# Kernel tuning notes

Hardware: AMD Instinct MI355X
Metric: run time of the kernel (lower is better)

## Reference

```python
import jax, jax.numpy as jnp
import numpy as np

_LOG2PI = float(np.log(2.0 * np.pi))


def setup_inputs() -> dict:
    key = jax.random.key(0)
    ks = jax.random.split(key, 9)
    B, T, S, A, O = 64, 128, 512, 16, 4096
    regime = jax.random.randint(ks[0], (B,), 0, 2).astype(jnp.float32)
    obs = jax.random.randint(ks[1], (T + 1, B), 0, O, dtype=jnp.int32)
    rewards = jax.random.normal(ks[2], (T + 1, B), jnp.float32)
    dones = jnp.zeros((T + 1, B), jnp.float32)
    actions = jax.random.randint(ks[3], (T, B), 0, A, dtype=jnp.int32)
    prior_logits = jax.random.normal(ks[4], (S,), jnp.float32)
    trans_logits = jax.random.normal(ks[5], (A, S, S), jnp.float32)
    obs_logits = jax.random.normal(ks[6], (S, O), jnp.float32)
    policy_logits = jax.random.normal(ks[7], (S, A), jnp.float32)
    r_mu = jax.random.normal(ks[8], (S,), jnp.float32)
    r_logsig = jnp.zeros((S,), jnp.float32)
    return {"regime": regime, "obs": obs, "rewards": rewards, "dones": dones,
            "actions": actions, "prior_logits": prior_logits,
            "trans_logits": trans_logits, "obs_logits": obs_logits,
            "policy_logits": policy_logits, "r_mu": r_mu, "r_logsig": r_logsig}


def _log_prob(regime, obs, rewards, dones, actions, prior_logits, trans_logits,
              obs_logits, policy_logits, r_mu, r_logsig):
    # normalized log-prob tables (tabular instantiation of AugmentedModel)
    log_prior = jax.nn.log_softmax(prior_logits)              # [S]
    log_trans = jax.nn.log_softmax(trans_logits, axis=-1)     # [A,S,S]
    log_obs = jax.nn.log_softmax(obs_logits, axis=-1)         # [S,O]
    log_pol = jax.nn.log_softmax(policy_logits, axis=-1)      # [S,A]
    lse = jax.scipy.special.logsumexp

    def emis(o, r):  # log q(o|s) + log q(r|s) -> [B,S]
        lo = log_obs.T[o]                                      # [B,S] gather
        lr = (-0.5 * (((r[:, None] - r_mu[None, :]) * jnp.exp(-r_logsig)[None, :]) ** 2)
              - r_logsig[None, :] - 0.5 * _LOG2PI)             # [B,S]
        return lo + lr

    def act_term(a, done):  # masked log q(a|s) -> [B,S]
        la = log_pol.T[a]                                      # [B,S]
        la = jnp.where((done == 1.0)[:, None], jnp.zeros_like(la), la)
        la = jnp.where((regime == 1.0)[:, None], jnp.zeros_like(la), la)
        return la

    T = actions.shape[0]
    B = regime.shape[0]

    # t = 0
    was_done = jnp.zeros((B,), rewards.dtype)
    done0 = dones[0]
    lq_sorda = log_prior[None, :] + emis(obs[0], rewards[0]) + act_term(actions[0], done0)
    lq_orda = lse(lq_sorda, axis=-1) * (1.0 - was_done)        # [B]
    log_prob = lq_orda
    lq_s_h = lq_sorda - lq_orda[:, None]
    # belief propagation through transition: [B,S,1] + [B,S,S] -> lse over prev state
    lq_snext_h = lse(lq_s_h[:, :, None] + log_trans[actions[0]], axis=1)

    def step(carry, xs):  # t = 1 .. T-1 (has an action)
        log_prob, was_done, lq_s_hprev = carry
        o, r, d, a = xs
        done = jnp.maximum(was_done, d)
        lq = lq_s_hprev + emis(o, r) + act_term(a, done)
        lq_orda = lse(lq, axis=-1) * (1.0 - was_done)
        log_prob = jnp.where(jnp.isinf(log_prob), log_prob, log_prob + lq_orda)
        lq_s_h = lq - lq_orda[:, None]
        lq_snext = lse(lq_s_h[:, :, None] + log_trans[a], axis=1)
        return (log_prob, done, lq_snext), None

    xs = (obs[1:T], rewards[1:T], dones[1:T], actions[1:T])
    (log_prob, was_done, lq_s_hprev), _ = jax.lax.scan(
        step, (log_prob, done0, lq_snext_h), xs)

    # final step t = T (no action term)
    lq = lq_s_hprev + emis(obs[T], rewards[T])
    lq_ord = lse(lq, axis=-1) * (1.0 - was_done)
    log_prob = jnp.where(jnp.isinf(log_prob), log_prob, log_prob + lq_ord)
    return log_prob


def reference(regime, obs, rewards, dones, actions, prior_logits, trans_logits,
              obs_logits, policy_logits, r_mu, r_logsig):
    return _log_prob(regime, obs, rewards, dones, actions, prior_logits,
                     trans_logits, obs_logits, policy_logits, r_mu, r_logsig)
```

## Files before the change

kernel.cpp:

```cpp
#include <hip/hip_runtime.h>
#include <math.h>

#define DI __device__ __forceinline__

constexpr int BB = 64;
constexpr int TT = 128;
constexpr int SS = 512;
constexpr int AA = 16;
constexpr int OO = 4096;
constexpr float LOG2PI = 1.8378770664093453f;
constexpr float LOG4096 = 8.317766166719343f;

typedef float f32x4 __attribute__((ext_vector_type(4)));

DI void lds_barrier() {
    asm volatile("s_waitcnt lgkmcnt(0)\n\ts_barrier" ::: "memory");
}

DI unsigned int f32_to_e4m3(float x) {
    unsigned int u = __float_as_uint(x);
    unsigned int lsb = (u >> 20) & 1u;
    unsigned int rounded = u + 0x7ffffu + lsb;
    int e8 = (int)(rounded >> 23) - 120;
    unsigned int m3 = (rounded >> 20) & 7u;
    unsigned int norm = ((unsigned int)e8 << 3) | m3;
    int sub = __float2int_rn(x * 512.0f);
    return (e8 <= 0) ? (unsigned int)sub : norm;
}

DI float bflyMax(float v) {
#pragma unroll
    for (int off = 32; off; off >>= 1) v = fmaxf(v, __shfl_xor(v, off));
    return v;
}
DI float bflySum(float v) {
#pragma unroll
    for (int off = 32; off; off >>= 1) v += __shfl_xor(v, off);
    return v;
}
DI float halfMax(float v) {
#pragma unroll
    for (int off = 16; off; off >>= 1) v = fmaxf(v, __shfl_xor(v, off));
    return v;
}
DI float halfSum(float v) {
#pragma unroll
    for (int off = 16; off; off >>= 1) v += __shfl_xor(v, off);
    return v;
}

template <int NW>
DI float blockMax(float v, float* wr) {
    v = bflyMax(v);
    const int lane = threadIdx.x & 63, wv = threadIdx.x >> 6;
    if (lane == 0) wr[wv] = v;
    __syncthreads();
    float r = wr[0];
#pragma unroll
    for (int i = 1; i < NW; ++i) r = fmaxf(r, wr[i]);
    __syncthreads();
    return r;
}
template <int NW>
DI float blockSum(float v, float* wr) {
    v = bflySum(v);
    const int lane = threadIdx.x & 63, wv = threadIdx.x >> 6;
    if (lane == 0) wr[wv] = v;
    __syncthreads();
    float r = wr[0];
#pragma unroll
    for (int i = 1; i < NW; ++i) r += wr[i];
    __syncthreads();
    return r;
}


__global__ __launch_bounds__(1024) void k_pack(const float* __restrict__ tl,
                                               unsigned char* __restrict__ PB) {
    __shared__ unsigned char lds[16384];
    const int a = blockIdx.x >> 4;
    const int kt = blockIdx.x & 15;
    const int tid = threadIdx.x;
    const int r = tid >> 5;
    const int nt = tid & 31;
    const int k = kt * 32 + r;
    const float* row = tl + ((size_t)a * SS + k) * SS + nt * 16;

    float x[16];
#pragma unroll
    for (int i = 0; i < 4; ++i) {
        float4 v = ((const float4*)row)[i];
        x[4 * i] = v.x; x[4 * i + 1] = v.y; x[4 * i + 2] = v.z; x[4 * i + 3] = v.w;
    }
    float mx = -INFINITY;
#pragma unroll
    for (int i = 0; i < 16; ++i) mx = fmaxf(mx, x[i]);
    mx = halfMax(mx);
    float e[16];
    float sm = 0.f;
#pragma unroll
    for (int i = 0; i < 16; ++i) { e[i] = __expf(x[i] - mx); sm += e[i]; }
    sm = halfSum(sm);
    const float scale = 256.0f / sm;

    const int base = (nt >> 1) * 1024 + ((r >> 3) * 16) * 16 + (nt & 1) * 8 + (r & 7);
#pragma unroll
    for (int i = 0; i < 16; ++i) {
        lds[base + i * 16] = (unsigned char)f32_to_e4m3(e[i] * scale);
    }
    __syncthreads();

    ulonglong2* dst = (ulonglong2*)(PB + (size_t)(a * 16 + kt) * 16384);
    dst[tid] = ((const ulonglong2*)lds)[tid];
}

__global__ __launch_bounds__(256) void k_obs_stats(const float* __restrict__ ol,
                                                   float* __restrict__ mo,
                                                   float* __restrict__ lo) {
    __shared__ float wr[4];
    const int s = blockIdx.x;
    const float* in = ol + (size_t)s * OO;
    const int tid = threadIdx.x;
    float mx = -INFINITY;
    for (int i = tid; i < OO; i += 256) mx = fmaxf(mx, in[i]);
    float m = blockMax<4>(mx, wr);
    float sm = 0.f;
    for (int i = tid; i < OO; i += 256) sm += __expf(in[i] - m);
    float sum = blockSum<4>(sm, wr);
    if (tid == 0) { mo[s] = m; lo[s] = __logf(sum); }
}

__global__ __launch_bounds__(256) void k_obsT(const float* __restrict__ ol,
                                              const float* __restrict__ mo,
                                              const float* __restrict__ lo,
                                              float* __restrict__ obsT) {
    __shared__ float tile[64][65];
    const int tO = blockIdx.x % (OO / 64);
    const int tS = blockIdx.x / (OO / 64);
    const int o0 = tO * 64, s0 = tS * 64;
    const int cc = threadIdx.x & 63, rr = threadIdx.x >> 6;
#pragma unroll
    for (int j = 0; j < 16; ++j) {
        int r = rr + j * 4;
        tile[r][cc] = ol[(size_t)(s0 + r) * OO + o0 + cc] - mo[s0 + r] - lo[s0 + r];
    }
    __syncthreads();
#pragma unroll
    for (int j = 0; j < 16; ++j) {
        int r = rr + j * 4;
        obsT[(size_t)(o0 + r) * SS + s0 + cc] = tile[cc][r];
    }
}

__global__ __launch_bounds__(512, 2) void k_main(
    const float* __restrict__ regime, const int* __restrict__ obs,
    const float* __restrict__ rewards, const float* __restrict__ dones,
    const int* __restrict__ actions, const float* __restrict__ prior_logits,
    const unsigned char* __restrict__ PB, const float* __restrict__ obsT,
    const float* __restrict__ policy_logits, const float* __restrict__ r_mu,
    const float* __restrict__ r_logsig, float* __restrict__ out) {
    __shared__ float wrm[8], wrs[8];
    __shared__ alignas(16) unsigned char p8[4 * 144 + 16];
    __shared__ int obs_l[TT + 1];
    __shared__ float rew_l[TT + 1];
    __shared__ float done_l[TT + 1];
    __shared__ int act_l[TT];

    const int b = blockIdx.x;
    const int tid = threadIdx.x;
    const int wv = tid >> 6, lane = tid & 63, quad = lane >> 4;
    const int s = tid;
    const int wvl16 = wv * 2048 + lane * 16;
    const int p8idx = ((s >> 3) & 3) * 144 + (s >> 5) * 8 + (s & 7);

    if (tid <= TT) {
        obs_l[tid] = obs[tid * BB + b];
        rew_l[tid] = rewards[tid * BB + b];
        done_l[tid] = dones[tid * BB + b];
        if (tid < TT) act_l[tid] = actions[tid * BB + b];
    }
    float la16[16];
    {
        const float4* pr4 = (const float4*)(policy_logits + (size_t)s * AA);
        float4 v0 = pr4[0], v1 = pr4[1], v2 = pr4[2], v3 = pr4[3];
        la16[0] = v0.x; la16[1] = v0.y; la16[2] = v0.z; la16[3] = v0.w;
        la16[4] = v1.x; la16[5] = v1.y; la16[6] = v1.z; la16[7] = v1.w;
        la16[8] = v2.x; la16[9] = v2.y; la16[10] = v2.z; la16[11] = v2.w;
        la16[12] = v3.x; la16[13] = v3.y; la16[14] = v3.z; la16[15] = v3.w;
        float mx = la16[0];
#pragma unroll
        for (int i = 1; i < 16; ++i) mx = fmaxf(mx, la16[i]);
        float sm = 0.f;
#pragma unroll
        for (int i = 0; i < 16; ++i) sm += __expf(la16[i] - mx);
        float ls = mx + __logf(sm);
#pragma unroll
        for (int i = 0; i < 16; ++i) la16[i] -= ls;
    }
    const float rm = r_mu[s];
    const float rls = r_logsig[s];
    const float inv_sig = __expf(-rls);
    const float reg = regime[b];

    float px = prior_logits[s];
    {
        float wm0 = bflyMax(px);
        if (lane == 0) wrm[wv] = wm0;
    }
    lds_barrier();
    float pm = wrm[0];
#pragma unroll
    for (int i = 1; i < 8; ++i) pm = fmaxf(pm, wrm[i]);
    {
        float ws0 = bflySum(__expf(px - pm));
        if (lane == 0) wrs[wv] = ws0;
    }
    lds_barrier();
    float psum = wrs[0];
#pragma unroll
    for (int i = 1; i < 8; ++i) psum += wrs[i];
    float base_reg = px - pm - __logf(psum);

    float obsv = obsT[(size_t)obs_l[0] * SS + s];

    float log_prob = 0.f;
    float was_done = 0.f;

    for (int t = 0; t < TT; ++t) {
        const float r = rew_l[t];
        const int a = __builtin_amdgcn_readfirstlane(act_l[t]);
        const float d = done_l[t];
        const float done = fmaxf(was_done, d);
        const unsigned char* Pw = PB + (size_t)a * (16 * 16384) + wvl16;

        ulonglong2 fA[16], fB[16];
#pragma unroll
        for (int c = 0; c < 16; ++c) {
            fA[c] = *(const ulonglong2*)(Pw + (size_t)c * 16384);
            fB[c] = *(const ulonglong2*)(Pw + (size_t)c * 16384 + 1024);
        }
        float obsv_next = obsT[(size_t)obs_l[t + 1] * SS + s];
        __builtin_amdgcn_sched_barrier(0);

        float diff = (r - rm) * inv_sig;
        float emis = obsv - 0.5f * diff * diff - rls - 0.5f * LOG2PI;
        float la = la16[0];
#pragma unroll
        for (int i = 1; i < 16; ++i) la = (a == i) ? la16[i] : la;
        if (done == 1.0f || reg == 1.0f) la = 0.f;
        float lq = base_reg + emis + la;

        float wmax = bflyMax(lq);
        if (lane == 0) wrm[wv] = wmax;
        lds_barrier();
        float m = wrm[0];
#pragma unroll
        for (int i = 1; i < 8; ++i) m = fmaxf(m, wrm[i]);

        float exv = __expf(lq - m);
        p8[p8idx] = (unsigned char)f32_to_e4m3(exv * 16.0f);
        float wsum = bflySum(exv);
        if (lane == 0) wrs[wv] = wsum;
        lds_barrier();
        float sum = wrs[0];
#pragma unroll
        for (int i = 1; i < 8; ++i) sum += wrs[i];
        float lse = m + __logf(sum);
        float lq_orda = lse * (1.0f - was_done);
        if (!isinf(log_prob)) log_prob += lq_orda;
        was_done = done;

        const float basev = m - lq_orda - LOG4096;
        f32x4 acc0 = {0.f, 0.f, 0.f, 0.f};
        f32x4 acc1 = {0.f, 0.f, 0.f, 0.f};
        f32x4 acc2 = {0.f, 0.f, 0.f, 0.f};
        f32x4 acc3 = {0.f, 0.f, 0.f, 0.f};

#define CHUNK(c)                                                                \
        {                                                                       \
            long af = *(const long long*)(p8 + quad * 144 + (c) * 8);           \
            acc0 = __builtin_amdgcn_mfma_f32_16x16x32_fp8_fp8((long)fA[(c)].x, af, acc0, 0, 0, 0); \
            acc1 = __builtin_amdgcn_mfma_f32_16x16x32_fp8_fp8((long)fA[(c)].y, af, acc1, 0, 0, 0); \
            acc2 = __builtin_amdgcn_mfma_f32_16x16x32_fp8_fp8((long)fB[(c)].x, af, acc2, 0, 0, 0); \
            acc3 = __builtin_amdgcn_mfma_f32_16x16x32_fp8_fp8((long)fB[(c)].y, af, acc3, 0, 0, 0); \
        }
        CHUNK(0)  CHUNK(1)  CHUNK(2)  CHUNK(3)
        CHUNK(4)  CHUNK(5)  CHUNK(6)  CHUNK(7)
        CHUNK(8)  CHUNK(9)  CHUNK(10) CHUNK(11)
        CHUNK(12) CHUNK(13) CHUNK(14) CHUNK(15)
#undef CHUNK

        float t0 = __shfl(acc0[0], lane & 15);
        float t1 = __shfl(acc1[0], lane & 15);
        float t2 = __shfl(acc2[0], lane & 15);
        float t3 = __shfl(acc3[0], lane & 15);
        float av = quad == 0 ? t0 : (quad == 1 ? t1 : (quad == 2 ? t2 : t3));
        base_reg = basev + __logf(av);
        obsv = obsv_next;
    }

    {
        const float r = rew_l[TT];
        float diff = (r - rm) * inv_sig;
        float emis = obsv - 0.5f * diff * diff - rls - 0.5f * LOG2PI;
        float lq = base_reg + emis;
        float wmax = bflyMax(lq);
        if (lane == 0) wrm[wv] = wmax;
        lds_barrier();
        float m = wrm[0];
#pragma unroll
        for (int i = 1; i < 8; ++i) m = fmaxf(m, wrm[i]);
        float wsum = bflySum(__expf(lq - m));
        if (lane == 0) wrs[wv] = wsum;
        lds_barrier();
        float sum = wrs[0];
#pragma unroll
        for (int i = 1; i < 8; ++i) sum += wrs[i];
        float lse = m + __logf(sum);
        float lq_ord = lse * (1.0f - was_done);
        if (!isinf(log_prob)) log_prob += lq_ord;
    }

    if (tid == 0) out[b] = log_prob;
}

extern "C" void kernel_launch(void* const* d_in, const int* in_sizes, int n_in,
                              void* d_out, int out_size, void* d_ws, size_t ws_size,
                              hipStream_t stream) {
    const float* regime = (const float*)d_in[0];
    const int* obs = (const int*)d_in[1];
    const float* rewards = (const float*)d_in[2];
    const float* dones = (const float*)d_in[3];
    const int* actions = (const int*)d_in[4];
    const float* prior_logits = (const float*)d_in[5];
    const float* trans_logits = (const float*)d_in[6];
    const float* obs_logits = (const float*)d_in[7];
    const float* policy_logits = (const float*)d_in[8];
    const float* r_mu = (const float*)d_in[9];
    const float* r_logsig = (const float*)d_in[10];
    float* out = (float*)d_out;

    char* ws = (char*)d_ws;
    unsigned char* PB = (unsigned char*)ws;
    float* obsT = (float*)(ws + (size_t)AA * SS * SS);
    float* mo = (float*)(ws + (size_t)AA * SS * SS + (size_t)OO * SS * 4);
    float* lo = mo + SS;

    k_pack<<<256, 1024, 0, stream>>>(trans_logits, PB);
    k_obs_stats<<<SS, 256, 0, stream>>>(obs_logits, mo, lo);
    k_obsT<<<(OO / 64) * (SS / 64), 256, 0, stream>>>(obs_logits, mo, lo, obsT);
    k_main<<<BB, 512, 0, stream>>>(regime, obs, rewards, dones, actions, prior_logits,
                                   PB, obsT, policy_logits, r_mu, r_logsig, out);
}
```

Before: 513.9 us.

## Stream transition-matrix loads with inline asm and staggered vmcnt waits per MFMA chunk

Replaces compiler-generated loads of the FP8 transition tiles with inline-asm global_load_dwordx4 issued in order. Before each MFMA chunk it waits only for that chunk's data using decreasing vmcnt counts, so matrix math can start before all 32 loads land. Per-step scalars (action, reward, done, next obs offset) are prefetched one step ahead so their latency overlaps the reduction barriers. This relies on exact vmcnt ordering: the obs load is issued first and counts toward the outstanding loads, and any compiler-inserted vector memory op would make the counts wrong.

Result: faster. 501.5 us (-2.4%).

```diff
diff --git a/kernel.cpp b/kernel.cpp
--- a/kernel.cpp
+++ b/kernel.cpp
@@ -12,6 +12,7 @@
 constexpr float LOG4096 = 8.317766166719343f;
 
 typedef float f32x4 __attribute__((ext_vector_type(4)));
+typedef long long ll2 __attribute__((ext_vector_type(2)));
 
 DI void lds_barrier() {
     asm volatile("s_waitcnt lgkmcnt(0)\n\ts_barrier" ::: "memory");
@@ -221,37 +222,56 @@
     for (int i = 1; i < 8; ++i) psum += wrs[i];
     float base_reg = px - pm - __logf(psum);
 
-    float obsv = obsT[(size_t)obs_l[0] * SS + s];
+    float obsv;
+    {
+        int ov0 = (obs_l[0] * SS + s) * 4;
+        asm volatile("global_load_dword %0, %1, %2"
+                     : "=v"(obsv) : "v"(ov0), "s"((const void*)obsT));
+        asm volatile("s_waitcnt vmcnt(0)");
+        __builtin_amdgcn_sched_barrier(0);
+    }
+    int a_cur = __builtin_amdgcn_readfirstlane(act_l[0]);
+    float r_cur = rew_l[0];
+    float d_cur = done_l[0];
+    int onx_cur = (obs_l[1] * SS + s) * 4;
 
     float log_prob = 0.f;
     float was_done = 0.f;
 
     for (int t = 0; t < TT; ++t) {
-        const float r = rew_l[t];
-        const int a = __builtin_amdgcn_readfirstlane(act_l[t]);
-        const float d = done_l[t];
-        const float done = fmaxf(was_done, d);
-        const unsigned char* Pw = PB + (size_t)a * (16 * 16384) + wvl16;
-
-        ulonglong2 fA[16], fB[16];
+        const unsigned char* PBa = PB + (size_t)a_cur * (16 * 16384);
+
+        float obsv_next;
+        asm volatile("global_load_dword %0, %1, %2"
+                     : "=v"(obsv_next) : "v"(onx_cur), "s"((const void*)obsT));
+        ll2 fA[16], fB[16];
 #pragma unroll
         for (int c = 0; c < 16; ++c) {
-            fA[c] = *(const ulonglong2*)(Pw + (size_t)c * 16384);
-            fB[c] = *(const ulonglong2*)(Pw + (size_t)c * 16384 + 1024);
+            asm volatile("global_load_dwordx4 %0, %2, %3\n\t"
+                         "global_load_dwordx4 %1, %2, %3 offset:1024"
+                         : "=v"(fA[c]), "=v"(fB[c])
+                         : "v"(wvl16), "s"((const void*)(PBa + (size_t)c * 16384)));
         }
-        float obsv_next = obsT[(size_t)obs_l[t + 1] * SS + s];
-        __builtin_amdgcn_sched_barrier(0);
-
-        float diff = (r - rm) * inv_sig;
+
+        const float done = fmaxf(was_done, d_cur);
+        float diff = (r_cur - rm) * inv_sig;
         float emis = obsv - 0.5f * diff * diff - rls - 0.5f * LOG2PI;
         float la = la16[0];
 #pragma unroll
-        for (int i = 1; i < 16; ++i) la = (a == i) ? la16[i] : la;
+        for (int i = 1; i < 16; ++i) la = (a_cur == i) ? la16[i] : la;
         if (done == 1.0f || reg == 1.0f) la = 0.f;
         float lq = base_reg + emis + la;
 
         float wmax = bflyMax(lq);
         if (lane == 0) wrm[wv] = wmax;
+
+        const int tn1 = (t + 1 < TT) ? (t + 1) : (TT - 1);
+        const int tn2 = (t + 2 <= TT) ? (t + 2) : TT;
+        int a_nxt = __builtin_amdgcn_readfirstlane(act_l[tn1]);
+        float r_nxt = rew_l[t + 1];
+        float d_nxt = done_l[t + 1];
+        int onx_nxt = (obs_l[tn2] * SS + s) * 4;
+
         lds_barrier();
         float m = wrm[0];
 #pragma unroll
@@ -271,23 +291,28 @@
         was_done = done;
 
         const float basev = m - lq_orda - LOG4096;
+        long long af16[16];
+#pragma unroll
+        for (int c = 0; c < 16; ++c)
+            af16[c] = *(const long long*)(p8 + quad * 144 + c * 8);
+
         f32x4 acc0 = {0.f, 0.f, 0.f, 0.f};
         f32x4 acc1 = {0.f, 0.f, 0.f, 0.f};
         f32x4 acc2 = {0.f, 0.f, 0.f, 0.f};
         f32x4 acc3 = {0.f, 0.f, 0.f, 0.f};
 
-#define CHUNK(c)                                                                \
-        {                                                                       \
-            long af = *(const long long*)(p8 + quad * 144 + (c) * 8);           \
-            acc0 = __builtin_amdgcn_mfma_f32_16x16x32_fp8_fp8((long)fA[(c)].x, af, acc0, 0, 0, 0); \
-            acc1 = __builtin_amdgcn_mfma_f32_16x16x32_fp8_fp8((long)fA[(c)].y, af, acc1, 0, 0, 0); \
-            acc2 = __builtin_amdgcn_mfma_f32_16x16x32_fp8_fp8((long)fB[(c)].x, af, acc2, 0, 0, 0); \
-            acc3 = __builtin_amdgcn_mfma_f32_16x16x32_fp8_fp8((long)fB[(c)].y, af, acc3, 0, 0, 0); \
-        }
-        CHUNK(0)  CHUNK(1)  CHUNK(2)  CHUNK(3)
-        CHUNK(4)  CHUNK(5)  CHUNK(6)  CHUNK(7)
-        CHUNK(8)  CHUNK(9)  CHUNK(10) CHUNK(11)
-        CHUNK(12) CHUNK(13) CHUNK(14) CHUNK(15)
+#define CHUNK(c, n)                                                             \
+        asm volatile("s_waitcnt vmcnt(" #n ")");                                \
+        __builtin_amdgcn_sched_barrier(0);                                      \
+        acc0 = __builtin_amdgcn_mfma_f32_16x16x32_fp8_fp8((long)fA[c].x, (long)af16[c], acc0, 0, 0, 0); \
+        acc1 = __builtin_amdgcn_mfma_f32_16x16x32_fp8_fp8((long)fA[c].y, (long)af16[c], acc1, 0, 0, 0); \
+        acc2 = __builtin_amdgcn_mfma_f32_16x16x32_fp8_fp8((long)fB[c].x, (long)af16[c], acc2, 0, 0, 0); \
+        acc3 = __builtin_amdgcn_mfma_f32_16x16x32_fp8_fp8((long)fB[c].y, (long)af16[c], acc3, 0, 0, 0);
+
+        CHUNK(0, 30)  CHUNK(1, 28)  CHUNK(2, 26)  CHUNK(3, 24)
+        CHUNK(4, 22)  CHUNK(5, 20)  CHUNK(6, 18)  CHUNK(7, 16)
+        CHUNK(8, 14)  CHUNK(9, 12)  CHUNK(10, 10) CHUNK(11, 8)
+        CHUNK(12, 6)  CHUNK(13, 4)  CHUNK(14, 2)  CHUNK(15, 0)
 #undef CHUNK
 
         float t0 = __shfl(acc0[0], lane & 15);
@@ -297,6 +322,7 @@
         float av = quad == 0 ? t0 : (quad == 1 ? t1 : (quad == 2 ? t2 : t3));
         base_reg = basev + __logf(av);
         obsv = obsv_next;
+        a_cur = a_nxt; r_cur = r_nxt; d_cur = d_nxt; onx_cur = onx_nxt;
     }
 
     {
```

## Add producer warps streaming transition tiles into LDS ring via async global-to-LDS loads

Applied to the files above, without the earlier changes.

Two extra producer wavefronts stream the fp8 transition-matrix chunks for each step into an 8-slot LDS ring using global_load_lds, with ready flags and a consumer counter for flow control. The eight compute wavefronts now read the B operand from LDS instead of issuing 32 global loads per step into registers. Hardware s_barrier is replaced by a software atomic-counter barrier among the compute waves only, so the producers are not blocked by it. The aim is to hide the per-step global-load latency on the serial recurrence. In exchange it adds spin-wait polling, a 128KB LDS footprint, and fragile cross-wave synchronisation.

Measured after the change: 718.9 us. 39.9% more time.

```diff
diff --git a/kernel.cpp b/kernel.cpp
--- a/kernel.cpp
+++ b/kernel.cpp
@@ -8,13 +8,16 @@
 constexpr int SS = 512;
 constexpr int AA = 16;
 constexpr int OO = 4096;
+constexpr int RING = 8;
 constexpr float LOG2PI = 1.8378770664093453f;
 constexpr float LOG4096 = 8.317766166719343f;
 
 typedef float f32x4 __attribute__((ext_vector_type(4)));
 
-DI void lds_barrier() {
-    asm volatile("s_waitcnt lgkmcnt(0)\n\ts_barrier" ::: "memory");
+typedef __attribute__((address_space(3))) unsigned int as3_u32;
+typedef __attribute__((address_space(1))) const unsigned int as1_u32;
+DI void dma1k(const unsigned char* g, unsigned char* l) {
+    __builtin_amdgcn_global_load_lds((as1_u32*)g, (as3_u32*)l, 16, 0, 0);
 }
 
 DI unsigned int f32_to_e4m3(float x) {
@@ -152,33 +155,80 @@
     }
 }
 
-__global__ __launch_bounds__(512, 2) void k_main(
+__global__ __launch_bounds__(640) void k_main(
     const float* __restrict__ regime, const int* __restrict__ obs,
     const float* __restrict__ rewards, const float* __restrict__ dones,
     const int* __restrict__ actions, const float* __restrict__ prior_logits,
     const unsigned char* __restrict__ PB, const float* __restrict__ obsT,
     const float* __restrict__ policy_logits, const float* __restrict__ r_mu,
     const float* __restrict__ r_logsig, float* __restrict__ out) {
+    __shared__ alignas(16) unsigned char ring[RING * 16384];
     __shared__ float wrm[8], wrs[8];
     __shared__ alignas(16) unsigned char p8[4 * 144 + 16];
     __shared__ int obs_l[TT + 1];
     __shared__ float rew_l[TT + 1];
     __shared__ float done_l[TT + 1];
     __shared__ int act_l[TT];
+    __shared__ unsigned ready[RING];
+    __shared__ unsigned cntC, barc;
 
     const int b = blockIdx.x;
     const int tid = threadIdx.x;
     const int wv = tid >> 6, lane = tid & 63, quad = lane >> 4;
-    const int s = tid;
-    const int wvl16 = wv * 2048 + lane * 16;
-    const int p8idx = ((s >> 3) & 3) * 144 + (s >> 5) * 8 + (s & 7);
-
+
+    if (tid == 0) { cntC = 0u; barc = 0u; }
+    if (tid < RING) ready[tid] = 0xFFFFFFFFu;
     if (tid <= TT) {
         obs_l[tid] = obs[tid * BB + b];
         rew_l[tid] = rewards[tid * BB + b];
         done_l[tid] = dones[tid * BB + b];
         if (tid < TT) act_l[tid] = actions[tid * BB + b];
     }
+    __syncthreads();
+
+    if (wv >= 8) {
+        const int wid = wv - 8;
+        for (int g = wid; g < 16 * TT; g += 2) {
+            const int t = g >> 4, c = g & 15;
+            const int a = __builtin_amdgcn_readfirstlane(act_l[t]);
+            if (g >= RING) {
+                const unsigned tgt = 8u * (unsigned)(g - RING + 1);
+                while (*(volatile unsigned*)&cntC < tgt)
+                    __builtin_amdgcn_s_sleep(1);
+            }
+            const unsigned char* gp =
+                PB + (size_t)a * (16 * 16384) + (size_t)c * 16384 + lane * 16;
+            unsigned char* lp = ring + (size_t)(g & (RING - 1)) * 16384;
+#pragma unroll
+            for (int seg = 0; seg < 16; ++seg)
+                dma1k(gp + seg * 1024, lp + seg * 1024);
+            asm volatile("s_waitcnt vmcnt(16)" ::: "memory");
+            __builtin_amdgcn_sched_barrier(0);
+            if (g >= 2 && lane == 0)
+                *(volatile unsigned*)&ready[(g - 2) & (RING - 1)] = (unsigned)(g - 2);
+        }
+        asm volatile("s_waitcnt vmcnt(0)" ::: "memory");
+        __builtin_amdgcn_sched_barrier(0);
+        if (lane == 0) {
+            const int gl = 16 * TT - 2 + wid;
+            *(volatile unsigned*)&ready[gl & (RING - 1)] = (unsigned)gl;
+        }
+        return;
+    }
+
+    const int s = tid;
+    const int p8idx = ((s >> 3) & 3) * 144 + (s >> 5) * 8 + (s & 7);
+    unsigned bep = 0;
+
+#define CBAR()                                                                  \
+    {                                                                           \
+        asm volatile("s_waitcnt lgkmcnt(0)" ::: "memory");                      \
+        if (lane == 0) atomicAdd(&barc, 1u);                                    \
+        bep += 8u;                                                              \
+        while (*(volatile unsigned*)&barc < bep) {}                             \
+        __builtin_amdgcn_sched_barrier(0);                                      \
+    }
+
     float la16[16];
     {
         const float4* pr4 = (const float4*)(policy_logits + (size_t)s * AA);
@@ -207,7 +257,7 @@
         float wm0 = bflyMax(px);
         if (lane == 0) wrm[wv] = wm0;
     }
-    lds_barrier();
+    CBAR();
     float pm = wrm[0];
 #pragma unroll
     for (int i = 1; i < 8; ++i) pm = fmaxf(pm, wrm[i]);
@@ -215,7 +265,7 @@
         float ws0 = bflySum(__expf(px - pm));
         if (lane == 0) wrs[wv] = ws0;
     }
-    lds_barrier();
+    CBAR();
     float psum = wrs[0];
 #pragma unroll
     for (int i = 1; i < 8; ++i) psum += wrs[i];
@@ -231,16 +281,7 @@
         const int a = __builtin_amdgcn_readfirstlane(act_l[t]);
         const float d = done_l[t];
         const float done = fmaxf(was_done, d);
-        const unsigned char* Pw = PB + (size_t)a * (16 * 16384) + wvl16;
-
-        ulonglong2 fA[16], fB[16];
-#pragma unroll
-        for (int c = 0; c < 16; ++c) {
-            fA[c] = *(const ulonglong2*)(Pw + (size_t)c * 16384);
-            fB[c] = *(const ulonglong2*)(Pw + (size_t)c * 16384 + 1024);
-        }
         float obsv_next = obsT[(size_t)obs_l[t + 1] * SS + s];
-        __builtin_amdgcn_sched_barrier(0);
 
         float diff = (r - rm) * inv_sig;
         float emis = obsv - 0.5f * diff * diff - rls - 0.5f * LOG2PI;
@@ -252,7 +293,7 @@
 
         float wmax = bflyMax(lq);
         if (lane == 0) wrm[wv] = wmax;
-        lds_barrier();
+        CBAR();
         float m = wrm[0];
 #pragma unroll
         for (int i = 1; i < 8; ++i) m = fmaxf(m, wrm[i]);
@@ -261,7 +302,7 @@
         p8[p8idx] = (unsigned char)f32_to_e4m3(exv * 16.0f);
         float wsum = bflySum(exv);
         if (lane == 0) wrs[wv] = wsum;
-        lds_barrier();
+        CBAR();
         float sum = wrs[0];
 #pragma unroll
         for (int i = 1; i < 8; ++i) sum += wrs[i];
@@ -271,18 +312,33 @@
         was_done = done;
 
         const float basev = m - lq_orda - LOG4096;
+        long long af16[16];
+#pragma unroll
+        for (int c = 0; c < 16; ++c)
+            af16[c] = *(const long long*)(p8 + quad * 144 + c * 8);
+
         f32x4 acc0 = {0.f, 0.f, 0.f, 0.f};
         f32x4 acc1 = {0.f, 0.f, 0.f, 0.f};
         f32x4 acc2 = {0.f, 0.f, 0.f, 0.f};
         f32x4 acc3 = {0.f, 0.f, 0.f, 0.f};
+        const int g0 = 16 * t;
 
 #define CHUNK(c)                                                                \
         {                                                                       \
-            long af = *(const long long*)(p8 + quad * 144 + (c) * 8);           \
-            acc0 = __builtin_amdgcn_mfma_f32_16x16x32_fp8_fp8((long)fA[(c)].x, af, acc0, 0, 0, 0); \
-            acc1 = __builtin_amdgcn_mfma_f32_16x16x32_fp8_fp8((long)fA[(c)].y, af, acc1, 0, 0, 0); \
-            acc2 = __builtin_amdgcn_mfma_f32_16x16x32_fp8_fp8((long)fB[(c)].x, af, acc2, 0, 0, 0); \
-            acc3 = __builtin_amdgcn_mfma_f32_16x16x32_fp8_fp8((long)fB[(c)].y, af, acc3, 0, 0, 0); \
+            const int g_ = g0 + (c);                                            \
+            while ((int)__hip_atomic_load(&ready[(c) & (RING - 1)],             \
+                                          __ATOMIC_ACQUIRE,                     \
+                                          __HIP_MEMORY_SCOPE_WORKGROUP) < g_) {}\
+            const unsigned char* sb =                                           \
+                ring + (size_t)((c) & (RING - 1)) * 16384 + wv * 2048 + lane * 16; \
+            ulonglong2 f0 = *(const ulonglong2*)(sb);                           \
+            ulonglong2 f1 = *(const ulonglong2*)(sb + 1024);                    \
+            acc0 = __builtin_amdgcn_mfma_f32_16x16x32_fp8_fp8((long)f0.x, (long)af16[c], acc0, 0, 0, 0); \
+            acc1 = __builtin_amdgcn_mfma_f32_16x16x32_fp8_fp8((long)f0.y, (long)af16[c], acc1, 0, 0, 0); \
+            acc2 = __builtin_amdgcn_mfma_f32_16x16x32_fp8_fp8((long)f1.x, (long)af16[c], acc2, 0, 0, 0); \
+            acc3 = __builtin_amdgcn_mfma_f32_16x16x32_fp8_fp8((long)f1.y, (long)af16[c], acc3, 0, 0, 0); \
+            __builtin_amdgcn_sched_barrier(0);                                  \
+            if (lane == 0) atomicAdd(&cntC, 1u);                                \
         }
         CHUNK(0)  CHUNK(1)  CHUNK(2)  CHUNK(3)
         CHUNK(4)  CHUNK(5)  CHUNK(6)  CHUNK(7)
@@ -306,13 +362,13 @@
         float lq = base_reg + emis;
         float wmax = bflyMax(lq);
         if (lane == 0) wrm[wv] = wmax;
-        lds_barrier();
+        CBAR();
         float m = wrm[0];
 #pragma unroll
         for (int i = 1; i < 8; ++i) m = fmaxf(m, wrm[i]);
         float wsum = bflySum(__expf(lq - m));
         if (lane == 0) wrs[wv] = wsum;
-        lds_barrier();
+        CBAR();
         float sum = wrs[0];
 #pragma unroll
         for (int i = 1; i < 8; ++i) sum += wrs[i];
@@ -320,6 +376,7 @@
         float lq_ord = lse * (1.0f - was_done);
         if (!isinf(log_prob)) log_prob += lq_ord;
     }
+#undef CBAR
 
     if (tid == 0) out[b] = log_prob;
 }
@@ -349,6 +406,6 @@
     k_pack<<<256, 1024, 0, stream>>>(trans_logits, PB);
     k_obs_stats<<<SS, 256, 0, stream>>>(obs_logits, mo, lo);
     k_obsT<<<(OO / 64) * (SS / 64), 256, 0, stream>>>(obs_logits, mo, lo, obsT);
-    k_main<<<BB, 512, 0, stream>>>(regime, obs, rewards, dones, actions, prior_logits,
+    k_main<<<BB, 640, 0, stream>>>(regime, obs, rewards, dones, actions, prior_logits,
                                    PB, obsT, policy_logits, r_mu, r_logsig, out);
 }
```

## Split per-step FP8 MFMA matvec across 16 waves with LDS exchange

Applied to the files above, without the earlier changes.

Doubles the main kernel's block to 1024 threads so each of 16 waves computes 32 output states per step instead of 64, halving the per-wave transition-matrix loads and MFMA chain. Only the first 512 threads do the emission/softmax work. The matvec results go through a new LDS buffer with an extra barrier per step. The policy log-softmax table moves from registers to LDS to free VGPRs for the larger block. This adds one barrier per timestep and idles half the threads during the reductions.

Result: slower. 540.5 us (+5.2%).

```diff
diff --git a/kernel.cpp b/kernel.cpp
--- a/kernel.cpp
+++ b/kernel.cpp
@@ -152,13 +152,15 @@
     }
 }
 
-__global__ __launch_bounds__(512, 2) void k_main(
+__global__ __launch_bounds__(1024) void k_main(
     const float* __restrict__ regime, const int* __restrict__ obs,
     const float* __restrict__ rewards, const float* __restrict__ dones,
     const int* __restrict__ actions, const float* __restrict__ prior_logits,
     const unsigned char* __restrict__ PB, const float* __restrict__ obsT,
     const float* __restrict__ policy_logits, const float* __restrict__ r_mu,
     const float* __restrict__ r_logsig, float* __restrict__ out) {
+    __shared__ float la_lds[AA * SS];
+    __shared__ float lqprev[SS];
     __shared__ float wrm[8], wrs[8];
     __shared__ alignas(16) unsigned char p8[4 * 144 + 16];
     __shared__ int obs_l[TT + 1];
@@ -170,8 +172,9 @@
     const int tid = threadIdx.x;
     const int wv = tid >> 6, lane = tid & 63, quad = lane >> 4;
     const int s = tid;
-    const int wvl16 = wv * 2048 + lane * 16;
-    const int p8idx = ((s >> 3) & 3) * 144 + (s >> 5) * 8 + (s & 7);
+    const bool isA = (tid < SS);
+    const int p8idx = ((tid >> 3) & 3) * 144 + ((tid >> 5) & 15) * 8 + (tid & 7);
+    const int wl16 = wv * 1024 + lane * 16;
 
     if (tid <= TT) {
         obs_l[tid] = obs[tid * BB + b];
@@ -179,9 +182,10 @@
         done_l[tid] = dones[tid * BB + b];
         if (tid < TT) act_l[tid] = actions[tid * BB + b];
     }
-    float la16[16];
-    {
+    float rm = 0.f, rls = 0.f, inv_sig = 0.f;
+    if (isA) {
         const float4* pr4 = (const float4*)(policy_logits + (size_t)s * AA);
+        float la16[16];
         float4 v0 = pr4[0], v1 = pr4[1], v2 = pr4[2], v3 = pr4[3];
         la16[0] = v0.x; la16[1] = v0.y; la16[2] = v0.z; la16[3] = v0.w;
         la16[4] = v1.x; la16[5] = v1.y; la16[6] = v1.z; la16[7] = v1.w;
@@ -195,33 +199,36 @@
         for (int i = 0; i < 16; ++i) sm += __expf(la16[i] - mx);
         float ls = mx + __logf(sm);
 #pragma unroll
-        for (int i = 0; i < 16; ++i) la16[i] -= ls;
-    }
-    const float rm = r_mu[s];
-    const float rls = r_logsig[s];
-    const float inv_sig = __expf(-rls);
+        for (int i = 0; i < 16; ++i) la_lds[i * SS + s] = la16[i] - ls;
+        rm = r_mu[s];
+        rls = r_logsig[s];
+        inv_sig = __expf(-rls);
+    }
     const float reg = regime[b];
 
-    float px = prior_logits[s];
+    float base_reg = 0.f;
     {
-        float wm0 = bflyMax(px);
-        if (lane == 0) wrm[wv] = wm0;
-    }
-    lds_barrier();
-    float pm = wrm[0];
-#pragma unroll
-    for (int i = 1; i < 8; ++i) pm = fmaxf(pm, wrm[i]);
-    {
-        float ws0 = bflySum(__expf(px - pm));
-        if (lane == 0) wrs[wv] = ws0;
-    }
-    lds_barrier();
-    float psum = wrs[0];
-#pragma unroll
-    for (int i = 1; i < 8; ++i) psum += wrs[i];
-    float base_reg = px - pm - __logf(psum);
-
-    float obsv = obsT[(size_t)obs_l[0] * SS + s];
+        float px = isA ? prior_logits[s] : 0.f;
+        if (isA) {
+            float wm0 = bflyMax(px);
+            if (lane == 0) wrm[wv] = wm0;
+        }
+        lds_barrier();
+        float pm = wrm[0];
+#pragma unroll
+        for (int i = 1; i < 8; ++i) pm = fmaxf(pm, wrm[i]);
+        if (isA) {
+            float ws0 = bflySum(__expf(px - pm));
+            if (lane == 0) wrs[wv] = ws0;
+        }
+        lds_barrier();
+        float psum = wrs[0];
+#pragma unroll
+        for (int i = 1; i < 8; ++i) psum += wrs[i];
+        if (isA) base_reg = px - pm - __logf(psum);
+    }
+
+    float obsv = isA ? obsT[(size_t)obs_l[0] * SS + s] : 0.f;
 
     float log_prob = 0.f;
     float was_done = 0.f;
@@ -231,36 +238,35 @@
         const int a = __builtin_amdgcn_readfirstlane(act_l[t]);
         const float d = done_l[t];
         const float done = fmaxf(was_done, d);
-        const unsigned char* Pw = PB + (size_t)a * (16 * 16384) + wvl16;
-
-        ulonglong2 fA[16], fB[16];
-#pragma unroll
-        for (int c = 0; c < 16; ++c) {
+
+        const unsigned char* Pw = PB + (size_t)a * (16 * 16384) + wl16;
+        ulonglong2 fA[16];
+#pragma unroll
+        for (int c = 0; c < 16; ++c)
             fA[c] = *(const ulonglong2*)(Pw + (size_t)c * 16384);
-            fB[c] = *(const ulonglong2*)(Pw + (size_t)c * 16384 + 1024);
-        }
-        float obsv_next = obsT[(size_t)obs_l[t + 1] * SS + s];
-        __builtin_amdgcn_sched_barrier(0);
-
-        float diff = (r - rm) * inv_sig;
-        float emis = obsv - 0.5f * diff * diff - rls - 0.5f * LOG2PI;
-        float la = la16[0];
-#pragma unroll
-        for (int i = 1; i < 16; ++i) la = (a == i) ? la16[i] : la;
-        if (done == 1.0f || reg == 1.0f) la = 0.f;
-        float lq = base_reg + emis + la;
-
-        float wmax = bflyMax(lq);
-        if (lane == 0) wrm[wv] = wmax;
+
+        float obsv_next = 0.f, lq = 0.f;
+        if (isA) {
+            obsv_next = obsT[(size_t)obs_l[t + 1] * SS + s];
+            float diff = (r - rm) * inv_sig;
+            float emis = obsv - 0.5f * diff * diff - rls - 0.5f * LOG2PI;
+            float la = la_lds[a * SS + s];
+            if (done == 1.0f || reg == 1.0f) la = 0.f;
+            lq = base_reg + emis + la;
+            float wmax = bflyMax(lq);
+            if (lane == 0) wrm[wv] = wmax;
+        }
         lds_barrier();
         float m = wrm[0];
 #pragma unroll
         for (int i = 1; i < 8; ++i) m = fmaxf(m, wrm[i]);
 
-        float exv = __expf(lq - m);
-        p8[p8idx] = (unsigned char)f32_to_e4m3(exv * 16.0f);
-        float wsum = bflySum(exv);
-        if (lane == 0) wrs[wv] = wsum;
+        if (isA) {
+            float exv = __expf(lq - m);
+            p8[p8idx] = (unsigned char)f32_to_e4m3(exv * 16.0f);
+            float wsum = bflySum(exv);
+            if (lane == 0) wrs[wv] = wsum;
+        }
         lds_barrier();
         float sum = wrs[0];
 #pragma unroll
@@ -273,45 +279,40 @@
         const float basev = m - lq_orda - LOG4096;
         f32x4 acc0 = {0.f, 0.f, 0.f, 0.f};
         f32x4 acc1 = {0.f, 0.f, 0.f, 0.f};
-        f32x4 acc2 = {0.f, 0.f, 0.f, 0.f};
-        f32x4 acc3 = {0.f, 0.f, 0.f, 0.f};
-
-#define CHUNK(c)                                                                \
-        {                                                                       \
-            long af = *(const long long*)(p8 + quad * 144 + (c) * 8);           \
-            acc0 = __builtin_amdgcn_mfma_f32_16x16x32_fp8_fp8((long)fA[(c)].x, af, acc0, 0, 0, 0); \
-            acc1 = __builtin_amdgcn_mfma_f32_16x16x32_fp8_fp8((long)fA[(c)].y, af, acc1, 0, 0, 0); \
-            acc2 = __builtin_amdgcn_mfma_f32_16x16x32_fp8_fp8((long)fB[(c)].x, af, acc2, 0, 0, 0); \
-            acc3 = __builtin_amdgcn_mfma_f32_16x16x32_fp8_fp8((long)fB[(c)].y, af, acc3, 0, 0, 0); \
-        }
-        CHUNK(0)  CHUNK(1)  CHUNK(2)  CHUNK(3)
-        CHUNK(4)  CHUNK(5)  CHUNK(6)  CHUNK(7)
-        CHUNK(8)  CHUNK(9)  CHUNK(10) CHUNK(11)
-        CHUNK(12) CHUNK(13) CHUNK(14) CHUNK(15)
-#undef CHUNK
-
-        float t0 = __shfl(acc0[0], lane & 15);
-        float t1 = __shfl(acc1[0], lane & 15);
-        float t2 = __shfl(acc2[0], lane & 15);
-        float t3 = __shfl(acc3[0], lane & 15);
-        float av = quad == 0 ? t0 : (quad == 1 ? t1 : (quad == 2 ? t2 : t3));
-        base_reg = basev + __logf(av);
+#pragma unroll
+        for (int c = 0; c < 16; ++c) {
+            long af = *(const long long*)(p8 + quad * 144 + c * 8);
+            acc0 = __builtin_amdgcn_mfma_f32_16x16x32_fp8_fp8((long)fA[c].x, af, acc0, 0, 0, 0);
+            acc1 = __builtin_amdgcn_mfma_f32_16x16x32_fp8_fp8((long)fA[c].y, af, acc1, 0, 0, 0);
+        }
+
+        if (lane < 16) {
+            lqprev[wv * 32 + lane]      = basev + __logf(acc0[0]);
+            lqprev[wv * 32 + 16 + lane] = basev + __logf(acc1[0]);
+        }
+        lds_barrier();
+        if (isA) base_reg = lqprev[s];
         obsv = obsv_next;
     }
 
     {
-        const float r = rew_l[TT];
-        float diff = (r - rm) * inv_sig;
-        float emis = obsv - 0.5f * diff * diff - rls - 0.5f * LOG2PI;
-        float lq = base_reg + emis;
-        float wmax = bflyMax(lq);
-        if (lane == 0) wrm[wv] = wmax;
+        float lq = 0.f;
+        if (isA) {
+            const float r = rew_l[TT];
+            float diff = (r - rm) * inv_sig;
+            float emis = obsv - 0.5f * diff * diff - rls - 0.5f * LOG2PI;
+            lq = base_reg + emis;
+            float wmax = bflyMax(lq);
+            if (lane == 0) wrm[wv] = wmax;
+        }
         lds_barrier();
         float m = wrm[0];
 #pragma unroll
         for (int i = 1; i < 8; ++i) m = fmaxf(m, wrm[i]);
-        float wsum = bflySum(__expf(lq - m));
-        if (lane == 0) wrs[wv] = wsum;
+        if (isA) {
+            float wsum = bflySum(__expf(lq - m));
+            if (lane == 0) wrs[wv] = wsum;
+        }
         lds_barrier();
         float sum = wrs[0];
 #pragma unroll
@@ -349,6 +350,6 @@
     k_pack<<<256, 1024, 0, stream>>>(trans_logits, PB);
     k_obs_stats<<<SS, 256, 0, stream>>>(obs_logits, mo, lo);
     k_obsT<<<(OO / 64) * (SS / 64), 256, 0, stream>>>(obs_logits, mo, lo, obsT);
-    k_main<<<BB, 512, 0, stream>>>(regime, obs, rewards, dones, actions, prior_logits,
-                                   PB, obsT, policy_logits, r_mu, r_logsig, out);
-}
+    k_main<<<BB, 1024, 0, stream>>>(regime, obs, rewards, dones, actions, prior_logits,
+                                    PB, obsT, policy_logits, r_mu, r_logsig, out);
+}
```
